# Performance work log

Hardware: AMD Instinct MI355X
Metric: run time of the kernel (lower is better)

## Reference

```python
import jax, jax.numpy as jnp
import numpy as np

N_TOKENS = 65536
D_MODEL = 256
D_HID = 256
N_EXPERTS = 8


def setup_inputs() -> dict:
    key = jax.random.key(0)
    ks = jax.random.split(key, 6)
    x = jax.random.normal(ks[0], (N_TOKENS, D_MODEL), dtype=jnp.float32)
    # gate Linear weight [E, d] (torch Linear stores [out, in]); small init like nn.Linear default scale
    wg = jax.random.normal(ks[1], (N_EXPERTS, D_MODEL), dtype=jnp.float32) * 0.06
    W1 = jax.random.normal(ks[2], (N_EXPERTS, D_MODEL, D_HID), dtype=jnp.float32) * 0.06
    b1 = jnp.zeros((N_EXPERTS, D_HID), dtype=jnp.float32)
    W2 = jax.random.normal(ks[3], (N_EXPERTS, D_HID, D_MODEL), dtype=jnp.float32) * 0.06
    b2 = jnp.zeros((N_EXPERTS, D_MODEL), dtype=jnp.float32)
    return {"x": x, "wg": wg, "W1": W1, "b1": b1, "W2": W2, "b2": b2}


def reference(x, wg, W1, b1, W2, b2):
    # Gate: logits = x @ wg.T ; softmax over experts ; top-1 gate value + assignment
    gates = jax.nn.softmax(x @ wg.T, axis=1)                  # [N, E]
    gate_val = jnp.max(gates, axis=1)                          # [N] == topk(k=1) values
    assign = jnp.argmax(gates, axis=1)                         # [N] expert id per token

    out = jnp.zeros_like(x)
    # Fixed small loop over experts (structural, not data-dim); each iter is one dense GEMM pair.
    for e in range(N_EXPERTS):
        h = jax.nn.relu(x @ W1[e] + b1[e])                     # [N, D_HID]
        y_e = h @ W2[e] + b2[e]                                # [N, D_MODEL]
        sel = (assign == e)[:, None]
        out = jnp.where(sel, y_e * gate_val[:, None], out)
    return out
```

## Files before the change

### kernel.cpp

```cpp
#include <hip/hip_runtime.h>
#include <hip/hip_bf16.h>
#include <math.h>

#define NTOK 65536
#define DMODEL 256
#define NEXP 8
#define CAP 65536
#define MAXTILES 1040
#define CSTRIDE 64

typedef __bf16 bf16_t;
typedef __bf16 bf16x8 __attribute__((ext_vector_type(8)));
typedef float f32x4 __attribute__((ext_vector_type(4)));

__device__ inline void async16(const void* g, void* l) {
  __builtin_amdgcn_global_load_lds(
      (const __attribute__((address_space(1))) unsigned int*)g,
      (__attribute__((address_space(3))) unsigned int*)l, 16, 0, 0);
}

__global__ __launch_bounds__(256) void gate_pack_kernel(
    const float* __restrict__ x, const float* __restrict__ wg,
    const float* __restrict__ W1, const float* __restrict__ W2,
    bf16_t* __restrict__ xb, float* __restrict__ gateval,
    int* __restrict__ counts, int* __restrict__ idxbuf,
    bf16_t* __restrict__ w1p, bf16_t* __restrict__ w2p) {
  __shared__ __align__(16) float xs[2][64 * 128];
  __shared__ double part[3][64][9];
  const int th = threadIdx.x;
  const int lane = th & 63;
  const int wv = th >> 6;
  const int tokbase = blockIdx.x * 128;
  const int xm = lane & 31;

  auto stage = [&](int u) {
#pragma unroll
    for (int i = 0; i < 8; ++i) {
      int p = i * 256 + th;
      int r = p >> 5, c = (p & 31) ^ (r & 31);
      async16(x + (size_t)(tokbase + (u >> 1) * 64 + r) * 256 + (u & 1) * 128 + c * 4,
              &xs[u & 1][(i * 256 + wv * 64) * 4]);
    }
  };

  stage(0);
#pragma unroll
  for (int jj = 0; jj < 4; ++jj) {
    int f = blockIdx.x * 4 + jj;
    int mat = f >> 10, e = (f >> 7) & 7, kf = (f >> 4) & 7, nt = f & 15;
    const float* src = (mat == 0 ? W1 : W2) + (size_t)e * 65536;
    bf16_t* dst = (mat == 0 ? w1p : w2p) + (((size_t)e * 8 + kf) * 16 + nt) * 512;
#pragma unroll
    for (int rep = 0; rep < 2; ++rep) {
      int kl = rep * 16 + (th >> 4), nl = th & 15;
      float v = src[(size_t)(kf * 32 + kl) * 256 + nt * 16 + nl];
      int lanep = nl + 16 * (kl >> 3), j = kl & 7;
      dst[lanep * 8 + j] = (bf16_t)v;
    }
  }
  __syncthreads();

  int bi0 = 0, bi1 = 0;
  double acc[8] = {0, 0, 0, 0, 0, 0, 0, 0};
#pragma unroll
  for (int u = 0; u < 4; ++u) {
    if (u < 3) stage(u + 1);
    const float* xh = xs[u & 1];
    const int h = u & 1, ps = u >> 1;
#pragma unroll
    for (int i = 0; i < 4; ++i) {
      int p = i * 256 + th;
      int r = p >> 4, cb = p & 15, mk = r & 31;
      f32x4 a = *(const f32x4*)&xh[r * 128 + (((2 * cb) ^ mk) * 4)];
      f32x4 b = *(const f32x4*)&xh[r * 128 + (((2 * cb + 1) ^ mk) * 4)];
      bf16x8 bv;
      bv[0] = (bf16_t)a[0]; bv[1] = (bf16_t)a[1];
      bv[2] = (bf16_t)a[2]; bv[3] = (bf16_t)a[3];
      bv[4] = (bf16_t)b[0]; bv[5] = (bf16_t)b[1];
      bv[6] = (bf16_t)b[2]; bv[7] = (bf16_t)b[3];
      *(bf16x8*)(xb + (size_t)(tokbase + ps * 64 + r) * 256 + h * 128 + cb * 8) = bv;
    }
#pragma unroll
    for (int g = 0; g < 4; ++g) {
      int c0 = wv * 8 + 2 * g;
      f32x4 a = *(const f32x4*)&xh[lane * 128 + ((c0 ^ xm) * 4)];
      f32x4 b = *(const f32x4*)&xh[lane * 128 + (((c0 + 1) ^ xm) * 4)];
      float xv[8] = {a[0], a[1], a[2], a[3], b[0], b[1], b[2], b[3]};
#pragma unroll
      for (int e = 0; e < 8; ++e) {
        const float* wge = wg + e * 256 + h * 128 + wv * 32 + g * 8;
        float s = 0.f;
#pragma unroll
        for (int j2 = 0; j2 < 8; ++j2) s = fmaf(xv[j2], wge[j2], s);
        acc[e] += (double)s;
      }
    }
    if (u & 1) {
      if (wv > 0) {
#pragma unroll
        for (int e = 0; e < 8; ++e) part[wv - 1][lane][e] = acc[e];
      }
      __syncthreads();
      if (wv == 0) {
        double a2[8];
#pragma unroll
        for (int e = 0; e < 8; ++e) a2[e] = acc[e];
#pragma unroll
        for (int s2 = 0; s2 < 3; ++s2)
#pragma unroll
          for (int e = 0; e < 8; ++e) a2[e] += part[s2][lane][e];
        double m = a2[0]; int bi = 0;
#pragma unroll
        for (int e = 1; e < 8; ++e) if (a2[e] > m) { m = a2[e]; bi = e; }
        float denom = 0.f;
#pragma unroll
        for (int e = 0; e < 8; ++e) denom += __expf((float)(a2[e] - m));
        gateval[tokbase + ps * 64 + lane] = 1.0f / denom;
        if (ps == 0) bi0 = bi; else bi1 = bi;
      }
#pragma unroll
      for (int e = 0; e < 8; ++e) acc[e] = 0.0;
      __syncthreads();
    } else {
      __syncthreads();
    }
  }

  if (wv == 0) {
    const unsigned long long below = (1ull << lane) - 1ull;
    int myc = 0;
#pragma unroll
    for (int e = 0; e < NEXP; ++e) {
      unsigned long long mk0 = __ballot(bi0 == e);
      unsigned long long mk1 = __ballot(bi1 == e);
      if (lane == e) myc = (int)__popcll(mk0) + (int)__popcll(mk1);
    }
    int mybase = 0;
    if (lane < NEXP) mybase = atomicAdd(&counts[lane * CSTRIDE], myc);
#pragma unroll
    for (int e = 0; e < NEXP; ++e) {
      unsigned long long mk0 = __ballot(bi0 == e);
      unsigned long long mk1 = __ballot(bi1 == e);
      int b0 = __shfl(mybase, e, 64);
      if (bi0 == e)
        idxbuf[e * CAP + b0 + (int)__popcll(mk0 & below)] = tokbase + lane;
      if (bi1 == e)
        idxbuf[e * CAP + b0 + (int)__popcll(mk0) + (int)__popcll(mk1 & below)] =
            tokbase + 64 + lane;
    }
  }
}

__global__ __launch_bounds__(512, 4) void moe_gemm_kernel(
    const bf16_t* __restrict__ xb, const bf16_t* __restrict__ w1p,
    const bf16_t* __restrict__ w2p, const float* __restrict__ b1,
    const float* __restrict__ b2, const float* __restrict__ gateval,
    const int* __restrict__ counts, const int* __restrict__ idxbuf,
    float* __restrict__ out) {
  int ex = -1, tm = 0, a2 = 0, cnte = 0;
#pragma unroll
  for (int e2 = 0; e2 < 8; ++e2) {
    int c = counts[e2 * CSTRIDE];
    int n = (c + 63) >> 6;
    if ((int)blockIdx.x >= a2 && (int)blockIdx.x < a2 + n) {
      ex = e2; tm = (int)blockIdx.x - a2; cnte = c;
    }
    a2 += n;
  }
  if (ex < 0) return;
  const int ccnt = cnte;
  __shared__ __align__(16) bf16_t ts[64 * 256];
  __shared__ int sidx[64];
  __shared__ float sgv[64];
  const int th = threadIdx.x;
  const int lane = th & 63, wv = th >> 6;
  const int lr = lane & 15, lq = lane >> 4;
  if (th < 64) {
    int r = tm * 64 + th;
    int t = idxbuf[ex * CAP + (r < ccnt ? r : ccnt - 1)];
    sidx[th] = t;
    sgv[th] = gateval[t];
  }
  __syncthreads();
#pragma unroll
  for (int i = 0; i < 4; ++i) {
    int p = i * 512 + th;
    int r = p >> 5, s = (p & 31) ^ (r & 31);
    async16(xb + (size_t)sidx[r] * 256 + s * 8, &ts[(i * 512 + wv * 64) * 8]);
  }
  __syncthreads();

  const bf16_t* w1e = w1p + (size_t)ex * 65536;
  {
    f32x4 acc[4][2] = {};
#pragma unroll
    for (int kk = 0; kk < 256; kk += 64) {
#pragma unroll
      for (int kb = 0; kb < 2; ++kb) {
        const int ks = (kk >> 3) + kb * 4 + lq;
        const int kf = (kk >> 5) + kb;
        bf16x8 af[4], bfr[2];
#pragma unroll
        for (int mi = 0; mi < 4; ++mi) {
          int r = mi * 16 + lr;
          af[mi] = *(const bf16x8*)&ts[(r * 32 + (ks ^ (r & 31))) * 8];
        }
#pragma unroll
        for (int ni = 0; ni < 2; ++ni)
          bfr[ni] = *(const bf16x8*)&w1e[((size_t)kf * 16 + wv * 2 + ni) * 512 + lane * 8];
#pragma unroll
        for (int mi = 0; mi < 4; ++mi)
#pragma unroll
          for (int ni = 0; ni < 2; ++ni)
            acc[mi][ni] = __builtin_amdgcn_mfma_f32_16x16x32_bf16(af[mi], bfr[ni], acc[mi][ni], 0, 0, 0);
      }
    }
    float b1v[2];
#pragma unroll
    for (int ni = 0; ni < 2; ++ni) b1v[ni] = b1[ex * 256 + wv * 32 + ni * 16 + lr];
    __syncthreads();
#pragma unroll
    for (int mi = 0; mi < 4; ++mi)
#pragma unroll
      for (int ni = 0; ni < 2; ++ni)
#pragma unroll
        for (int rr = 0; rr < 4; ++rr) {
          int m = mi * 16 + lq * 4 + rr;
          int n = wv * 32 + ni * 16 + lr;
          float v = acc[mi][ni][rr] + b1v[ni];
          v = v > 0.f ? v : 0.f;
          ts[(m * 32 + ((n >> 3) ^ (m & 31))) * 8 + (n & 7)] = (bf16_t)v;
        }
  }
  __syncthreads();

  const bf16_t* w2e = w2p + (size_t)ex * 65536;
  {
    f32x4 acc[4][2] = {};
#pragma unroll
    for (int kk = 0; kk < 256; kk += 64) {
#pragma unroll
      for (int kb = 0; kb < 2; ++kb) {
        const int ks = (kk >> 3) + kb * 4 + lq;
        const int kf = (kk >> 5) + kb;
        bf16x8 af[4], bfr[2];
#pragma unroll
        for (int mi = 0; mi < 4; ++mi) {
          int r = mi * 16 + lr;
          af[mi] = *(const bf16x8*)&ts[(r * 32 + (ks ^ (r & 31))) * 8];
        }
#pragma unroll
        for (int ni = 0; ni < 2; ++ni)
          bfr[ni] = *(const bf16x8*)&w2e[((size_t)kf * 16 + wv * 2 + ni) * 512 + lane * 8];
#pragma unroll
        for (int mi = 0; mi < 4; ++mi)
#pragma unroll
          for (int ni = 0; ni < 2; ++ni)
            acc[mi][ni] = __builtin_amdgcn_mfma_f32_16x16x32_bf16(af[mi], bfr[ni], acc[mi][ni], 0, 0, 0);
      }
    }
    float b2v[2];
#pragma unroll
    for (int ni = 0; ni < 2; ++ni) b2v[ni] = b2[ex * 256 + wv * 32 + ni * 16 + lr];
    __syncthreads();
    float* wb = (float*)&ts[0] + wv * 1024;
#pragma unroll
    for (int bt = 0; bt < 2; ++bt) {
#pragma unroll
      for (int mi2 = 0; mi2 < 2; ++mi2) {
        const int mi = bt * 2 + mi2;
#pragma unroll
        for (int ni = 0; ni < 2; ++ni)
#pragma unroll
          for (int rr = 0; rr < 4; ++rr) {
            int lm = mi2 * 16 + lq * 4 + rr;
            int lc = ni * 16 + lr;
            int m = mi * 16 + lq * 4 + rr;
            float v = (acc[mi][ni][rr] + b2v[ni]) * sgv[m];
            int slot = ((lc >> 2) + (lm & 7)) & 7;
            wb[lm * 32 + slot * 4 + (lc & 3)] = v;
          }
      }
#pragma unroll
      for (int rd = 0; rd < 4; ++rd) {
        int lm = rd * 8 + (lane >> 3);
        int kk2 = lane & 7;
        int slot = (kk2 + (lm & 7)) & 7;
        f32x4 v = *(const f32x4*)&wb[lm * 32 + slot * 4];
        int m = bt * 32 + lm;
        int row = tm * 64 + m;
        if (row < ccnt)
          *(f32x4*)&out[(size_t)sidx[m] * 256 + wv * 32 + kk2 * 4] = v;
      }
    }
  }
}

extern "C" void kernel_launch(void* const* d_in, const int* in_sizes, int n_in,
                              void* d_out, int out_size, void* d_ws, size_t ws_size,
                              hipStream_t stream) {
  (void)in_sizes; (void)n_in; (void)out_size; (void)ws_size;
  const float* x  = (const float*)d_in[0];
  const float* wg = (const float*)d_in[1];
  const float* W1 = (const float*)d_in[2];
  const float* b1 = (const float*)d_in[3];
  const float* W2 = (const float*)d_in[4];
  const float* b2 = (const float*)d_in[5];
  float* out = (float*)d_out;

  char* ws = (char*)d_ws;
  size_t off = 0;
  auto alloc = [&](size_t bytes) {
    void* p = ws + off;
    off += (bytes + 255) & ~(size_t)255;
    return p;
  };
  bf16_t* xb     = (bf16_t*)alloc((size_t)NTOK * DMODEL * 2);
  bf16_t* w1p    = (bf16_t*)alloc((size_t)NEXP * 256 * 256 * 2);
  bf16_t* w2p    = (bf16_t*)alloc((size_t)NEXP * 256 * 256 * 2);
  int*    idxbuf = (int*)alloc((size_t)NEXP * CAP * 4);
  float*  gv     = (float*)alloc((size_t)NTOK * 4);
  int*    counts = (int*)alloc((size_t)NEXP * CSTRIDE * 4);

  hipMemsetAsync(counts, 0, (size_t)NEXP * CSTRIDE * 4, stream);
  hipLaunchKernelGGL(gate_pack_kernel, dim3(NTOK / 128), dim3(256), 0, stream,
                     x, wg, W1, W2, xb, gv, counts, idxbuf, w1p, w2p);
  hipLaunchKernelGGL(moe_gemm_kernel, dim3(MAXTILES), dim3(512), 0, stream,
                     xb, w1p, w2p, b1, b2, gv, counts, idxbuf, out);
}
```

Before: 173.5 us.

## Read gathered token rows straight from global and write output directly

The first GEMM now loads its A operand from global memory per MFMA fragment using per-lane gathered row ids, instead of first staging the 64 gathered rows into LDS with async loads. The epilogue also stops transposing through LDS and writes scalar fp32 values directly to the scattered output rows, which removes two barriers. Every wave now reloads the same x rows from global or L2, and the output stores become 4-byte scattered writes rather than coalesced 16-byte vectors. Both changes increase memory traffic and transaction count.

```diff
diff --git a/kernel.cpp b/kernel.cpp
--- a/kernel.cpp
+++ b/kernel.cpp
@@ -169,7 +169,7 @@
   }
   if (ex < 0) return;
   const int ccnt = cnte;
-  __shared__ __align__(16) bf16_t ts[64 * 256];
+  __shared__ __align__(16) bf16_t hs[64 * 256];
   __shared__ int sidx[64];
   __shared__ float sgv[64];
   const int th = threadIdx.x;
@@ -182,13 +182,9 @@
     sgv[th] = gateval[t];
   }
   __syncthreads();
-#pragma unroll
-  for (int i = 0; i < 4; ++i) {
-    int p = i * 512 + th;
-    int r = p >> 5, s = (p & 31) ^ (r & 31);
-    async16(xb + (size_t)sidx[r] * 256 + s * 8, &ts[(i * 512 + wv * 64) * 8]);
-  }
-  __syncthreads();
+  int rowid[4];
+#pragma unroll
+  for (int mi = 0; mi < 4; ++mi) rowid[mi] = sidx[mi * 16 + lr];
 
   const bf16_t* w1e = w1p + (size_t)ex * 65536;
   {
@@ -197,14 +193,11 @@
     for (int kk = 0; kk < 256; kk += 64) {
 #pragma unroll
       for (int kb = 0; kb < 2; ++kb) {
-        const int ks = (kk >> 3) + kb * 4 + lq;
         const int kf = (kk >> 5) + kb;
         bf16x8 af[4], bfr[2];
 #pragma unroll
-        for (int mi = 0; mi < 4; ++mi) {
-          int r = mi * 16 + lr;
-          af[mi] = *(const bf16x8*)&ts[(r * 32 + (ks ^ (r & 31))) * 8];
-        }
+        for (int mi = 0; mi < 4; ++mi)
+          af[mi] = *(const bf16x8*)&xb[(size_t)rowid[mi] * 256 + kk + kb * 32 + lq * 8];
 #pragma unroll
         for (int ni = 0; ni < 2; ++ni)
           bfr[ni] = *(const bf16x8*)&w1e[((size_t)kf * 16 + wv * 2 + ni) * 512 + lane * 8];
@@ -218,7 +211,6 @@
     float b1v[2];
 #pragma unroll
     for (int ni = 0; ni < 2; ++ni) b1v[ni] = b1[ex * 256 + wv * 32 + ni * 16 + lr];
-    __syncthreads();
 #pragma unroll
     for (int mi = 0; mi < 4; ++mi)
 #pragma unroll
@@ -229,7 +221,7 @@
           int n = wv * 32 + ni * 16 + lr;
           float v = acc[mi][ni][rr] + b1v[ni];
           v = v > 0.f ? v : 0.f;
-          ts[(m * 32 + ((n >> 3) ^ (m & 31))) * 8 + (n & 7)] = (bf16_t)v;
+          hs[(m * 32 + ((n >> 3) ^ (m & 31))) * 8 + (n & 7)] = (bf16_t)v;
         }
   }
   __syncthreads();
@@ -247,7 +239,7 @@
 #pragma unroll
         for (int mi = 0; mi < 4; ++mi) {
           int r = mi * 16 + lr;
-          af[mi] = *(const bf16x8*)&ts[(r * 32 + (ks ^ (r & 31))) * 8];
+          af[mi] = *(const bf16x8*)&hs[(r * 32 + (ks ^ (r & 31))) * 8];
         }
 #pragma unroll
         for (int ni = 0; ni < 2; ++ni)
@@ -262,37 +254,22 @@
     float b2v[2];
 #pragma unroll
     for (int ni = 0; ni < 2; ++ni) b2v[ni] = b2[ex * 256 + wv * 32 + ni * 16 + lr];
-    __syncthreads();
-    float* wb = (float*)&ts[0] + wv * 1024;
-#pragma unroll
-    for (int bt = 0; bt < 2; ++bt) {
-#pragma unroll
-      for (int mi2 = 0; mi2 < 2; ++mi2) {
-        const int mi = bt * 2 + mi2;
-#pragma unroll
-        for (int ni = 0; ni < 2; ++ni)
-#pragma unroll
-          for (int rr = 0; rr < 4; ++rr) {
-            int lm = mi2 * 16 + lq * 4 + rr;
-            int lc = ni * 16 + lr;
-            int m = mi * 16 + lq * 4 + rr;
-            float v = (acc[mi][ni][rr] + b2v[ni]) * sgv[m];
-            int slot = ((lc >> 2) + (lm & 7)) & 7;
-            wb[lm * 32 + slot * 4 + (lc & 3)] = v;
+#pragma unroll
+    for (int mi = 0; mi < 4; ++mi)
+#pragma unroll
+      for (int rr = 0; rr < 4; ++rr) {
+        int m = mi * 16 + lq * 4 + rr;
+        int row = tm * 64 + m;
+        if (row < ccnt) {
+          int tk = sidx[m];
+          float g = sgv[m];
+#pragma unroll
+          for (int ni = 0; ni < 2; ++ni) {
+            int n = wv * 32 + ni * 16 + lr;
+            out[(size_t)tk * 256 + n] = (acc[mi][ni][rr] + b2v[ni]) * g;
           }
-      }
-#pragma unroll
-      for (int rd = 0; rd < 4; ++rd) {
-        int lm = rd * 8 + (lane >> 3);
-        int kk2 = lane & 7;
-        int slot = (kk2 + (lm & 7)) & 7;
-        f32x4 v = *(const f32x4*)&wb[lm * 32 + slot * 4];
-        int m = bt * 32 + lm;
-        int row = tm * 64 + m;
-        if (row < ccnt)
-          *(f32x4*)&out[(size_t)sidx[m] * 256 + wv * 32 + kk2 * 4] = v;
-      }
-    }
+        }
+      }
   }
 }
 
```

Result: slower. 194.0 us (+11.8%).
